# Kernel tuning notes

Hardware: AMD Instinct MI355X
Metric: run time of the kernel (lower is better)

## Reference

```python
import jax, jax.numpy as jnp
import numpy as np

B, L, C, D = 8, 8192, 256, 256


def setup_inputs() -> dict:
    key = jax.random.key(0)
    ks = jax.random.split(key, 13)
    bound = 1.0 / np.sqrt(C)

    def W(k):
        return jax.random.uniform(k, (C, D), jnp.float32, -bound, bound)

    def b(k):
        return jax.random.uniform(k, (D,), jnp.float32, -bound, bound)

    return {
        "xs": jax.random.normal(ks[0], (B, L, C), jnp.float32),
        # forward-direction params
        "Wh1": W(ks[1]), "bh1": b(ks[2]),
        "Wz1": W(ks[3]), "bz1": b(ks[4]),
        "Ws1": W(ks[5]), "bs1": b(ks[6]),
        "h01": jnp.zeros((1, 1, D), jnp.float32),
        # backward-direction params
        "Wh_1": W(ks[7]), "bh_1": b(ks[8]),
        "Wz_1": W(ks[9]), "bz_1": b(ks[10]),
        "Ws_1": W(ks[11]), "bs_1": b(ks[12]),
        "h0_1": jnp.zeros((1, 1, D), jnp.float32),
    }


def _gru_scan(z, h_tilde, h0):
    """h[t] = z[t]*h_tilde[t] + (1-z[t])*h[t-1], h[-1]=h0. Parallel over time
    via associative scan on the affine maps h -> a*h + b."""
    a = 1.0 - z            # [B, L, D]
    b = z * h_tilde        # [B, L, D]

    def combine(c1, c2):
        a1, b1 = c1
        a2, b2 = c2
        return a1 * a2, a2 * b1 + b2

    A, Bc = jax.lax.associative_scan(combine, (a, b), axis=1)
    return Bc + A * h0     # broadcast h0 [1,1,D]


def reference(xs, Wh1, bh1, Wz1, bz1, Ws1, bs1, h01,
              Wh_1, bh_1, Wz_1, bz_1, Ws_1, bs_1, h0_1):
    sig = jax.nn.sigmoid
    # forward direction
    hf = _gru_scan(sig(xs @ Wz1 + bz1), xs @ Wh1 + bh1, h01) * sig(xs @ Ws1 + bs1)
    # backward direction: reverse time, scan, reverse back
    zr = sig(xs @ Wz_1 + bz_1)
    hr = xs @ Wh_1 + bh_1
    hb = _gru_scan(zr[:, ::-1], hr[:, ::-1], h0_1)[:, ::-1] * sig(xs @ Ws_1 + bs_1)
    return hf + hb
```

## Files before the change

kernel.cpp:

```cpp
#include <hip/hip_runtime.h>
#include <hip/hip_bf16.h>

typedef unsigned short u16;

#define BDIM 8
#define LDIM 8192
#define KDIM 256
#define DDIM 256
#define MTOT 65536
#define NDIM 1536
#define TCH  32
#define NCH  256
#define NSUP 16


typedef float floatx4 __attribute__((ext_vector_type(4)));
typedef short bf16x8 __attribute__((ext_vector_type(8)));
typedef unsigned int u32x4 __attribute__((ext_vector_type(4)));
typedef unsigned int u32x2 __attribute__((ext_vector_type(2)));

__device__ __forceinline__ u16 f2bf(float f) {
  union { __hip_bfloat16 h; u16 u; } c;
  c.h = __float2bfloat16(f);
  return c.u;
}
__device__ __forceinline__ float bf2f(u16 u) {
  union { unsigned int i; float f; } c;
  c.i = ((unsigned int)u) << 16;
  return c.f;
}
__device__ __forceinline__ float sigmoidf_fast(float x) {
  return __builtin_amdgcn_rcpf(1.0f + __expf(-x));
}
__device__ __forceinline__ void gll16(const u16* g, u16* l) {
  __builtin_amdgcn_global_load_lds((const __attribute__((address_space(1))) void*)g,
                                   (__attribute__((address_space(3))) void*)l, 16, 0, 0);
}

__global__ void prep_conv(const float* __restrict__ Wh1, const float* __restrict__ Wz1,
                          const float* __restrict__ Ws1, const float* __restrict__ Wh_1,
                          const float* __restrict__ Wz_1, const float* __restrict__ Ws_1,
                          const float* __restrict__ bh1, const float* __restrict__ bz1,
                          const float* __restrict__ bs1, const float* __restrict__ bh_1,
                          const float* __restrict__ bz_1, const float* __restrict__ bs_1,
                          u16* __restrict__ WcatT, float* __restrict__ bcat,
                          const float* __restrict__ xs, u16* __restrict__ Abf) {
  if (blockIdx.x < NDIM) {
    const int n = blockIdx.x;
    const int k = threadIdx.x;
    const int nn = n & 63;
    const int p = (n & ~63) | ((nn & 15) << 2) | (nn >> 4);
    const int dir = p / 768, r = p % 768;
    int d; const float* W; const float* bb;
    if (r < 512) {
      d = r >> 1;
      if (r & 1) { W = dir ? Wz_1 : Wz1; bb = dir ? bz_1 : bz1; }
      else       { W = dir ? Wh_1 : Wh1; bb = dir ? bh_1 : bh1; }
    } else {
      d = r - 512;
      W = dir ? Ws_1 : Ws1; bb = dir ? bs_1 : bs1;
    }
    WcatT[(size_t)n * KDIM + k] = f2bf(W[k * DDIM + d]);
    if (k == 0) bcat[p] = bb[d];
  } else {
    const int cb = blockIdx.x - NDIM;
#pragma unroll
    for (int pass = 0; pass < 4; ++pass) {
      size_t i = ((size_t)(pass * 2048 + cb) * 256 + threadIdx.x) * 8;
      const float4* s = (const float4*)(xs + i);
      float4 f0 = s[0], f1 = s[1];
      union { u16 u[8]; u32x4 v; } t;
      t.u[0] = f2bf(f0.x); t.u[1] = f2bf(f0.y); t.u[2] = f2bf(f0.z); t.u[3] = f2bf(f0.w);
      t.u[4] = f2bf(f1.x); t.u[5] = f2bf(f1.y); t.u[6] = f2bf(f1.z); t.u[7] = f2bf(f1.w);
      *(u32x4*)(Abf + i) = t.v;
    }
  }
}

__global__ __launch_bounds__(256) void gemm_kernel(const u16* __restrict__ Abf,
                                                   const u16* __restrict__ WcatT,
                                                   const float* __restrict__ bcat,
                                                   u16* __restrict__ G,
                                                   float* __restrict__ Acc,
                                                   float* __restrict__ Bcc) {
  __shared__ __align__(16) u16 sm[16384];
  u16* As = sm;
  u16* Bs = sm + 8192;
  const int tid = threadIdx.x;
  const int lane = tid & 63, wave = tid >> 6;
  const int wm = wave >> 1, wn = wave & 1;
  const int q = lane >> 4, r = lane & 15;

  const int xcd = blockIdx.x & 7;
  const int li  = blockIdx.x >> 3;
  const int mt  = xcd * 64 + li / 12;
  const int nt  = li % 12;
  const int m0 = mt * 128, n0 = nt * 128;

  const u16* gA[4]; const u16* gB[4]; u16* lA[4]; u16* lB[4];
#pragma unroll
  for (int j = 0; j < 4; j++) {
    const int bi = wave * 256 + j * 64 + lane;
    const int row = bi >> 3;
    const int kq = (bi & 7) ^ (row & 7);
    gA[j] = Abf   + (size_t)(m0 + row) * KDIM + kq * 8;
    gB[j] = WcatT + (size_t)(n0 + row) * KDIM + kq * 8;
    lA[j] = As + bi * 8;
    lB[j] = Bs + bi * 8;
  }

  floatx4 acc[4][4];
  floatx4 z4 = {0.f, 0.f, 0.f, 0.f};
#pragma unroll
  for (int i = 0; i < 4; i++)
#pragma unroll
    for (int j = 0; j < 4; j++) acc[i][j] = z4;

  for (int k0 = 0; k0 < KDIM; k0 += 64) {
#pragma unroll
    for (int j = 0; j < 4; j++) { gll16(gA[j] + k0, lA[j]); gll16(gB[j] + k0, lB[j]); }
    __syncthreads();
#pragma unroll
    for (int kk = 0; kk < 2; kk++) {
      bf16x8 af[4], bv[4];
#pragma unroll
      for (int i = 0; i < 4; i++) {
        const int row = wm * 64 + i * 16 + r;
        af[i] = *(const bf16x8*)(As + (row * 8 + ((kk * 4 + q) ^ (row & 7))) * 8);
      }
#pragma unroll
      for (int j = 0; j < 4; j++) {
        const int row = wn * 64 + j * 16 + r;
        bv[j] = *(const bf16x8*)(Bs + (row * 8 + ((kk * 4 + q) ^ (row & 7))) * 8);
      }
#pragma unroll
      for (int i = 0; i < 4; i++)
#pragma unroll
        for (int j = 0; j < 4; j++)
          acc[i][j] = __builtin_amdgcn_mfma_f32_16x16x32_bf16(af[i], bv[j], acc[i][j], 0, 0, 0);
    }
    __syncthreads();
  }

  const int pcol = wn * 64 + (r << 2);
  const float4 bv4 = *(const float4*)(bcat + n0 + pcol);
  const int hz = (n0 % 768) < 512;

  if (hz) {
#pragma unroll
    for (int i = 0; i < 4; i++) {
#pragma unroll
      for (int reg = 0; reg < 4; reg++) {
        const int lrow = wm * 64 + i * 16 + q * 4 + reg;
        union { u16 u[4]; u32x2 v; } t;
        t.u[0] = f2bf(acc[i][0][reg] + bv4.x);
        t.u[1] = f2bf(acc[i][1][reg] + bv4.y);
        t.u[2] = f2bf(acc[i][2][reg] + bv4.z);
        t.u[3] = f2bf(acc[i][3][reg] + bv4.w);
        *(u32x2*)(sm + lrow * 128 + pcol) = t.v;
      }
    }

    __syncthreads();

#pragma unroll
    for (int p = 0; p < 8; p++) {
      const int idx = p * 2048 + tid * 8;
      const int row = idx >> 7, col = idx & 127;
      const u32x4 v = *(const u32x4*)(sm + idx);
      *(u32x4*)(G + (size_t)(m0 + row) * NDIM + n0 + col) = v;
    }

    const int cc = wave;
    const int dd = lane;
    const int dirn = n0 / 768;
    const int dbase = (n0 % 768) >> 1;
    const int bb = m0 >> 13;
    const int c0 = (m0 & 8191) >> 5;
    float h = 0.f, P = 1.f;
#pragma unroll 8
    for (int i = 0; i < TCH; ++i) {
      const int tl = dirn ? (TCH - 1 - i) : i;
      const unsigned int hzv = *(const unsigned int*)(sm + (cc * 32 + tl) * 128 + dd * 2);
      const float z = sigmoidf_fast(bf2f((u16)(hzv >> 16)));
      const float a = 1.f - z;
      h = fmaf(a, h, z * bf2f((u16)(hzv & 0xffffu)));
      P *= a;
    }
    const size_t u = (size_t)dirn * 2048 + (size_t)bb * 256 + (size_t)(c0 + cc);
    Acc[u * 256 + dbase + dd] = P;
    Bcc[u * 256 + dbase + dd] = h;
  } else {
#pragma unroll
    for (int i = 0; i < 4; i++) {
#pragma unroll
      for (int reg = 0; reg < 4; reg++) {
        const int lrow = wm * 64 + i * 16 + q * 4 + reg;
        union { u16 u[4]; u32x2 v; } t;
        t.u[0] = f2bf(acc[i][0][reg] + bv4.x);
        t.u[1] = f2bf(acc[i][1][reg] + bv4.y);
        t.u[2] = f2bf(acc[i][2][reg] + bv4.z);
        t.u[3] = f2bf(acc[i][3][reg] + bv4.w);
        *(u32x2*)(G + (size_t)(m0 + lrow) * NDIM + n0 + pcol) = t.v;
      }
    }
  }
}

__global__ __launch_bounds__(256) void scan_phaseB1(float* __restrict__ Acc,
                                                    float* __restrict__ Bcc,
                                                    float* __restrict__ Asum,
                                                    float* __restrict__ Bsum) {
  const int d = threadIdx.x;
  const int s   = blockIdx.x & 15;
  const int b   = (blockIdx.x >> 4) & 7;
  const int dir = blockIdx.x >> 7;
  const size_t ubase = ((size_t)dir * BDIM + b) * NCH;
  float a[16], bb[16];
#pragma unroll
  for (int i = 0; i < 16; ++i) {
    const int c = dir ? (NCH - 1 - (s * 16 + i)) : (s * 16 + i);
    const size_t idx = (ubase + c) * DDIM + d;
    a[i] = Acc[idx]; bb[i] = Bcc[idx];
  }
  float A = 1.f, Bv = 0.f;
#pragma unroll
  for (int i = 0; i < 16; ++i) {
    const int c = dir ? (NCH - 1 - (s * 16 + i)) : (s * 16 + i);
    const size_t idx = (ubase + c) * DDIM + d;
    Acc[idx] = A; Bcc[idx] = Bv;
    Bv = fmaf(a[i], Bv, bb[i]);
    A  = a[i] * A;
  }
  const size_t sidx = (((size_t)dir * BDIM + b) * NSUP + s) * DDIM + d;
  Asum[sidx] = A; Bsum[sidx] = Bv;
}

__global__ void scan_phaseB2(const float* __restrict__ Asum, const float* __restrict__ Bsum,
                             const float* __restrict__ h01, const float* __restrict__ h0_1,
                             float* __restrict__ Hsup) {
  const int d = threadIdx.x, b = blockIdx.x, dir = blockIdx.y;
  float h = dir ? h0_1[d] : h01[d];
  const size_t base = ((size_t)dir * BDIM + b) * NSUP;
  float A[16], Bv[16];
#pragma unroll
  for (int s = 0; s < 16; ++s) {
    A[s]  = Asum[(base + s) * DDIM + d];
    Bv[s] = Bsum[(base + s) * DDIM + d];
  }
#pragma unroll
  for (int s = 0; s < 16; ++s) {
    Hsup[(base + s) * DDIM + d] = h;
    h = fmaf(A[s], h, Bv[s]);
  }
}

__global__ __launch_bounds__(256) void scan_phaseC(const u16* __restrict__ G,
                                                   const float* __restrict__ Acc,
                                                   const float* __restrict__ Bcc,
                                                   const float* __restrict__ Hsup,
                                                   float* __restrict__ out) {
  __shared__ float obuf[TCH * 256];
  const int c = blockIdx.x & 255, b = blockIdx.x >> 8;
  const int dir = threadIdx.x >> 7;
  const int ld  = threadIdx.x & 127;
  const int d0 = ld * 2;
  const int u = dir * 2048 + b * 256 + c;
  const int sp = dir ? ((NCH - 1 - c) >> 4) : (c >> 4);
  const float2 hs = *(const float2*)(Hsup + ((((size_t)dir * BDIM + b) * NSUP + sp) * DDIM) + d0);
  const float2 ap = *(const float2*)(Acc + (size_t)u * 256 + d0);
  const float2 bp = *(const float2*)(Bcc + (size_t)u * 256 + d0);
  float h0 = fmaf(ap.x, hs.x, bp.x);
  float h1 = fmaf(ap.y, hs.y, bp.y);
  const u16* ghz = G + (size_t)b * LDIM * NDIM + dir * 768 + d0 * 2;
  const u16* gs  = G + (size_t)b * LDIM * NDIM + dir * 768 + 512 + d0;

#pragma unroll
  for (int i = 0; i < 16; ++i) {
    const int tl = dir ? (TCH - 1 - i) : i;
    const int t = c * TCH + tl;
    const uint2 hz4 = *(const uint2*)(ghz + (size_t)t * NDIM);
    const unsigned int s2 = *(const unsigned int*)(gs + (size_t)t * NDIM);
    const float z0 = sigmoidf_fast(bf2f((u16)(hz4.x >> 16)));
    const float z1 = sigmoidf_fast(bf2f((u16)(hz4.y >> 16)));
    h0 = fmaf(1.f - z0, h0, z0 * bf2f((u16)(hz4.x & 0xffffu)));
    h1 = fmaf(1.f - z1, h1, z1 * bf2f((u16)(hz4.y & 0xffffu)));
    float2 o;
    o.x = h0 * sigmoidf_fast(bf2f((u16)(s2 & 0xffffu)));
    o.y = h1 * sigmoidf_fast(bf2f((u16)(s2 >> 16)));
    *(float2*)(obuf + tl * 256 + d0) = o;
  }

  __syncthreads();

#pragma unroll
  for (int i = 16; i < 32; ++i) {
    const int tl = dir ? (TCH - 1 - i) : i;
    const int t = c * TCH + tl;
    const uint2 hz4 = *(const uint2*)(ghz + (size_t)t * NDIM);
    const unsigned int s2 = *(const unsigned int*)(gs + (size_t)t * NDIM);
    const float z0 = sigmoidf_fast(bf2f((u16)(hz4.x >> 16)));
    const float z1 = sigmoidf_fast(bf2f((u16)(hz4.y >> 16)));
    h0 = fmaf(1.f - z0, h0, z0 * bf2f((u16)(hz4.x & 0xffffu)));
    h1 = fmaf(1.f - z1, h1, z1 * bf2f((u16)(hz4.y & 0xffffu)));
    const float o0 = h0 * sigmoidf_fast(bf2f((u16)(s2 & 0xffffu)));
    const float o1 = h1 * sigmoidf_fast(bf2f((u16)(s2 >> 16)));
    const float2 other = *(const float2*)(obuf + tl * 256 + d0);
    float2 res;
    res.x = o0 + other.x;
    res.y = o1 + other.y;
    *(float2*)(out + ((size_t)b * LDIM + t) * DDIM + d0) = res;
  }
}

extern "C" void kernel_launch(void* const* d_in, const int* in_sizes, int n_in,
                              void* d_out, int out_size, void* d_ws, size_t ws_size,
                              hipStream_t stream) {
  const float* xs   = (const float*)d_in[0];
  const float* Wh1  = (const float*)d_in[1];
  const float* bh1  = (const float*)d_in[2];
  const float* Wz1  = (const float*)d_in[3];
  const float* bz1  = (const float*)d_in[4];
  const float* Ws1  = (const float*)d_in[5];
  const float* bs1  = (const float*)d_in[6];
  const float* h01  = (const float*)d_in[7];
  const float* Wh_1 = (const float*)d_in[8];
  const float* bh_1 = (const float*)d_in[9];
  const float* Wz_1 = (const float*)d_in[10];
  const float* bz_1 = (const float*)d_in[11];
  const float* Ws_1 = (const float*)d_in[12];
  const float* bs_1 = (const float*)d_in[13];
  const float* h0_1 = (const float*)d_in[14];
  float* out = (float*)d_out;

  char* ws = (char*)d_ws;
  u16* WcatT = (u16*)ws;   ws += (size_t)NDIM * KDIM * 2;
  float* bcat = (float*)ws; ws += (size_t)NDIM * 4;
  u16* Abf = (u16*)ws;     ws += (size_t)MTOT * KDIM * 2;
  u16* G = (u16*)ws;       ws += (size_t)MTOT * NDIM * 2;

  const size_t sumElems = (size_t)2 * BDIM * NCH * DDIM;
  const size_t supElems = (size_t)2 * BDIM * NSUP * DDIM;
  float* Acc  = (float*)ws; ws += sumElems * 4;
  float* Bcc  = (float*)ws; ws += sumElems * 4;
  float* Asum = (float*)ws; ws += supElems * 4;
  float* Bsum = (float*)ws; ws += supElems * 4;
  float* Hsup = (float*)ws; ws += supElems * 4;
  if ((size_t)(ws - (char*)d_ws) > ws_size) return;

  prep_conv<<<dim3(NDIM + 2048), dim3(256), 0, stream>>>(
      Wh1, Wz1, Ws1, Wh_1, Wz_1, Ws_1, bh1, bz1, bs1, bh_1, bz_1, bs_1,
      WcatT, bcat, xs, Abf);
  gemm_kernel<<<dim3(6144), dim3(256), 0, stream>>>(Abf, WcatT, bcat, G, Acc, Bcc);
  scan_phaseB1<<<dim3(256), dim3(DDIM), 0, stream>>>(Acc, Bcc, Asum, Bsum);
  scan_phaseB2<<<dim3(BDIM, 2), dim3(DDIM), 0, stream>>>(Asum, Bsum, h01, h0_1, Hsup);
  scan_phaseC<<<dim3(2048), dim3(256), 0, stream>>>(G, Acc, Bcc, Hsup, out);
}
```

Measured before the change: 269.6 us.

## Fold super-chunk prefix scan into phase C and batch gate loads

Removes the scan_phaseB2 kernel and its Hsup buffer. Each phase C block now recomputes the carry-in for its super-chunk by serially combining up to 15 Asum/Bsum entries. It also hoists the 16 gate loads per half into register arrays ahead of the recurrence so the memory loads can overlap. This saves one kernel launch and a tiny serial kernel, at the cost of redundant prefix work per block and higher register pressure.

Result: no change. 270.8 us, median of 2 (+0.4%).

```diff
diff --git a/kernel.cpp b/kernel.cpp
--- a/kernel.cpp
+++ b/kernel.cpp
@@ -236,80 +236,89 @@
   Asum[sidx] = A; Bsum[sidx] = Bv;
 }
 
-__global__ void scan_phaseB2(const float* __restrict__ Asum, const float* __restrict__ Bsum,
-                             const float* __restrict__ h01, const float* __restrict__ h0_1,
-                             float* __restrict__ Hsup) {
-  const int d = threadIdx.x, b = blockIdx.x, dir = blockIdx.y;
-  float h = dir ? h0_1[d] : h01[d];
-  const size_t base = ((size_t)dir * BDIM + b) * NSUP;
-  float A[16], Bv[16];
-#pragma unroll
-  for (int s = 0; s < 16; ++s) {
-    A[s]  = Asum[(base + s) * DDIM + d];
-    Bv[s] = Bsum[(base + s) * DDIM + d];
-  }
-#pragma unroll
-  for (int s = 0; s < 16; ++s) {
-    Hsup[(base + s) * DDIM + d] = h;
-    h = fmaf(A[s], h, Bv[s]);
-  }
-}
-
 __global__ __launch_bounds__(256) void scan_phaseC(const u16* __restrict__ G,
                                                    const float* __restrict__ Acc,
                                                    const float* __restrict__ Bcc,
-                                                   const float* __restrict__ Hsup,
+                                                   const float* __restrict__ Asum,
+                                                   const float* __restrict__ Bsum,
+                                                   const float* __restrict__ h01,
+                                                   const float* __restrict__ h0_1,
                                                    float* __restrict__ out) {
   __shared__ float obuf[TCH * 256];
   const int c = blockIdx.x & 255, b = blockIdx.x >> 8;
   const int dir = threadIdx.x >> 7;
   const int ld  = threadIdx.x & 127;
   const int d0 = ld * 2;
+
+  const int sp = dir ? ((NCH - 1 - c) >> 4) : (c >> 4);
+  const float2 hh = dir ? *(const float2*)(h0_1 + d0) : *(const float2*)(h01 + d0);
+  float ha = hh.x, hb = hh.y;
+  const size_t sbase = ((size_t)dir * BDIM + b) * NSUP;
+  for (int s = 0; s < sp; ++s) {
+    const float2 As2 = *(const float2*)(Asum + (sbase + s) * DDIM + d0);
+    const float2 Bs2 = *(const float2*)(Bsum + (sbase + s) * DDIM + d0);
+    ha = fmaf(As2.x, ha, Bs2.x);
+    hb = fmaf(As2.y, hb, Bs2.y);
+  }
   const int u = dir * 2048 + b * 256 + c;
-  const int sp = dir ? ((NCH - 1 - c) >> 4) : (c >> 4);
-  const float2 hs = *(const float2*)(Hsup + ((((size_t)dir * BDIM + b) * NSUP + sp) * DDIM) + d0);
   const float2 ap = *(const float2*)(Acc + (size_t)u * 256 + d0);
   const float2 bp = *(const float2*)(Bcc + (size_t)u * 256 + d0);
-  float h0 = fmaf(ap.x, hs.x, bp.x);
-  float h1 = fmaf(ap.y, hs.y, bp.y);
+  float h0 = fmaf(ap.x, ha, bp.x);
+  float h1 = fmaf(ap.y, hb, bp.y);
+
   const u16* ghz = G + (size_t)b * LDIM * NDIM + dir * 768 + d0 * 2;
   const u16* gs  = G + (size_t)b * LDIM * NDIM + dir * 768 + 512 + d0;
 
-#pragma unroll
-  for (int i = 0; i < 16; ++i) {
-    const int tl = dir ? (TCH - 1 - i) : i;
-    const int t = c * TCH + tl;
-    const uint2 hz4 = *(const uint2*)(ghz + (size_t)t * NDIM);
-    const unsigned int s2 = *(const unsigned int*)(gs + (size_t)t * NDIM);
-    const float z0 = sigmoidf_fast(bf2f((u16)(hz4.x >> 16)));
-    const float z1 = sigmoidf_fast(bf2f((u16)(hz4.y >> 16)));
-    h0 = fmaf(1.f - z0, h0, z0 * bf2f((u16)(hz4.x & 0xffffu)));
-    h1 = fmaf(1.f - z1, h1, z1 * bf2f((u16)(hz4.y & 0xffffu)));
-    float2 o;
-    o.x = h0 * sigmoidf_fast(bf2f((u16)(s2 & 0xffffu)));
-    o.y = h1 * sigmoidf_fast(bf2f((u16)(s2 >> 16)));
-    *(float2*)(obuf + tl * 256 + d0) = o;
+  {
+    uint2 hzr[16]; unsigned int sr[16];
+#pragma unroll
+    for (int i = 0; i < 16; ++i) {
+      const int tl = dir ? (TCH - 1 - i) : i;
+      const int t = c * TCH + tl;
+      hzr[i] = *(const uint2*)(ghz + (size_t)t * NDIM);
+      sr[i]  = *(const unsigned int*)(gs + (size_t)t * NDIM);
+    }
+#pragma unroll
+    for (int i = 0; i < 16; ++i) {
+      const int tl = dir ? (TCH - 1 - i) : i;
+      const float z0 = sigmoidf_fast(bf2f((u16)(hzr[i].x >> 16)));
+      const float z1 = sigmoidf_fast(bf2f((u16)(hzr[i].y >> 16)));
+      h0 = fmaf(1.f - z0, h0, z0 * bf2f((u16)(hzr[i].x & 0xffffu)));
+      h1 = fmaf(1.f - z1, h1, z1 * bf2f((u16)(hzr[i].y & 0xffffu)));
+      float2 o;
+      o.x = h0 * sigmoidf_fast(bf2f((u16)(sr[i] & 0xffffu)));
+      o.y = h1 * sigmoidf_fast(bf2f((u16)(sr[i] >> 16)));
+      *(float2*)(obuf + tl * 256 + d0) = o;
+    }
   }
 
   __syncthreads();
 
-#pragma unroll
-  for (int i = 16; i < 32; ++i) {
-    const int tl = dir ? (TCH - 1 - i) : i;
-    const int t = c * TCH + tl;
-    const uint2 hz4 = *(const uint2*)(ghz + (size_t)t * NDIM);
-    const unsigned int s2 = *(const unsigned int*)(gs + (size_t)t * NDIM);
-    const float z0 = sigmoidf_fast(bf2f((u16)(hz4.x >> 16)));
-    const float z1 = sigmoidf_fast(bf2f((u16)(hz4.y >> 16)));
-    h0 = fmaf(1.f - z0, h0, z0 * bf2f((u16)(hz4.x & 0xffffu)));
-    h1 = fmaf(1.f - z1, h1, z1 * bf2f((u16)(hz4.y & 0xffffu)));
-    const float o0 = h0 * sigmoidf_fast(bf2f((u16)(s2 & 0xffffu)));
-    const float o1 = h1 * sigmoidf_fast(bf2f((u16)(s2 >> 16)));
-    const float2 other = *(const float2*)(obuf + tl * 256 + d0);
-    float2 res;
-    res.x = o0 + other.x;
-    res.y = o1 + other.y;
-    *(float2*)(out + ((size_t)b * LDIM + t) * DDIM + d0) = res;
+  {
+    uint2 hzr[16]; unsigned int sr[16];
+#pragma unroll
+    for (int i = 0; i < 16; ++i) {
+      const int tl = dir ? (TCH - 1 - (16 + i)) : (16 + i);
+      const int t = c * TCH + tl;
+      hzr[i] = *(const uint2*)(ghz + (size_t)t * NDIM);
+      sr[i]  = *(const unsigned int*)(gs + (size_t)t * NDIM);
+    }
+#pragma unroll
+    for (int i = 0; i < 16; ++i) {
+      const int tl = dir ? (TCH - 1 - (16 + i)) : (16 + i);
+      const int t = c * TCH + tl;
+      const float z0 = sigmoidf_fast(bf2f((u16)(hzr[i].x >> 16)));
+      const float z1 = sigmoidf_fast(bf2f((u16)(hzr[i].y >> 16)));
+      h0 = fmaf(1.f - z0, h0, z0 * bf2f((u16)(hzr[i].x & 0xffffu)));
+      h1 = fmaf(1.f - z1, h1, z1 * bf2f((u16)(hzr[i].y & 0xffffu)));
+      const float o0 = h0 * sigmoidf_fast(bf2f((u16)(sr[i] & 0xffffu)));
+      const float o1 = h1 * sigmoidf_fast(bf2f((u16)(sr[i] >> 16)));
+      const float2 other = *(const float2*)(obuf + tl * 256 + d0);
+      float2 res;
+      res.x = o0 + other.x;
+      res.y = o1 + other.y;
+      *(float2*)(out + ((size_t)b * LDIM + t) * DDIM + d0) = res;
+    }
   }
 }
 
@@ -345,7 +354,6 @@
   float* Bcc  = (float*)ws; ws += sumElems * 4;
   float* Asum = (float*)ws; ws += supElems * 4;
   float* Bsum = (float*)ws; ws += supElems * 4;
-  float* Hsup = (float*)ws; ws += supElems * 4;
   if ((size_t)(ws - (char*)d_ws) > ws_size) return;
 
   prep_conv<<<dim3(NDIM + 2048), dim3(256), 0, stream>>>(
@@ -353,6 +361,5 @@
       WcatT, bcat, xs, Abf);
   gemm_kernel<<<dim3(6144), dim3(256), 0, stream>>>(Abf, WcatT, bcat, G, Acc, Bcc);
   scan_phaseB1<<<dim3(256), dim3(DDIM), 0, stream>>>(Acc, Bcc, Asum, Bsum);
-  scan_phaseB2<<<dim3(BDIM, 2), dim3(DDIM), 0, stream>>>(Asum, Bsum, h01, h0_1, Hsup);
-  scan_phaseC<<<dim3(2048), dim3(256), 0, stream>>>(G, Acc, Bcc, Hsup, out);
-}
+  scan_phaseC<<<dim3(2048), dim3(256), 0, stream>>>(G, Acc, Bcc, Asum, Bsum, h01, h0_1, out);
+}
```
